# Kernel optimization log

Measured on AMD Instinct MI355X. Metric: run time of the kernel, lower is better.

The kernel has to match this reference:

```python
import jax, jax.numpy as jnp
import numpy as np

D_MODEL = 1024
NUM_HEADS = 16
SEG = 512            # segment_size
DIL = 4              # dilation_rate
HEAD_DIM = D_MODEL // NUM_HEADS


def setup_inputs() -> dict:
    key = jax.random.key(0)
    ks = jax.random.split(key, 5)
    B, S = 4, 4096
    sc = D_MODEL ** -0.5  # keep projected activations O(1) so softmax is not saturated
    def w(k):
        return jax.random.normal(k, (D_MODEL, D_MODEL), jnp.float32) * sc
    z = jnp.zeros((D_MODEL,), jnp.float32)
    return {
        "x": jax.random.normal(ks[0], (B, S, D_MODEL), jnp.float32),
        "Wq": w(ks[1]), "bq": z,
        "Wk": w(ks[2]), "bk": z,
        "Wv": w(ks[3]), "bv": z,
        "Wo": w(ks[4]), "bo": z,
    }


def reference(x, Wq, bq, Wk, bk, Wv, bv, Wo, bo):
    B, S, D = x.shape
    H, hd, seg, r = NUM_HEADS, HEAD_DIM, SEG, DIL
    scaling = hd ** -0.5

    Q = x @ Wq + bq
    K = x @ Wk + bk
    V = x @ Wv + bv

    pad = (-S) % seg
    if pad:
        Q = jnp.pad(Q, ((0, 0), (0, pad), (0, 0)))
        K = jnp.pad(K, ((0, 0), (0, pad), (0, 0)))
        V = jnp.pad(V, ((0, 0), (0, pad), (0, 0)))
    n = (S + pad) // seg          # num_segments
    sd = seg // r                 # dilated positions per segment per head

    # [B, n, sd, r, H, hd]: position within segment = t*r + offset
    def split(t):
        return t.reshape(B, n, sd, r, H, hd)

    offs = jnp.arange(H) % r      # per-head dilation offset sj = j % r
    hidx = jnp.arange(H)
    # vectorized per-head dilated gather -> [B, n, sd, H, hd]
    Qs = split(Q)[:, :, :, offs, hidx, :]
    Ks = split(K)[:, :, :, offs, hidx, :]
    Vs = split(V)[:, :, :, offs, hidx, :]

    # diagonal q.k score per dilated position, softmax over the segment's dilated positions
    scores = jnp.einsum('bnshd,bnshd->bnsh', Qs, Ks) * scaling
    probs = jax.nn.softmax(scores, axis=2)
    attn = probs[..., None] * Vs  # [B, n, sd, H, hd]

    # scatter back to each head's dilated positions; other positions stay zero
    out = jnp.zeros((B, n, sd, r, H, hd), x.dtype)
    out = out.at[:, :, :, offs, hidx, :].set(attn)
    out = out.reshape(B, n * seg, D)[:, :S]
    return out @ Wo + bo
```

## Files before the change

kernel.cpp:

```cpp
#include <hip/hip_runtime.h>
#include <hip/hip_bf16.h>

typedef unsigned short u16;
typedef unsigned int u32;
typedef __attribute__((ext_vector_type(8))) __bf16 bf16x8;
typedef __attribute__((ext_vector_type(4))) float f32x4;

#define NB 4
#define SQ 4096
#define DM 1024
#define RPC 4096
#define S4 (4 * DM)

#define VMCNT(n) asm volatile("s_waitcnt vmcnt(" #n ")" ::: "memory")
#define LGKM0()  asm volatile("s_waitcnt lgkmcnt(0)" ::: "memory")
#define BARRIER() asm volatile("s_barrier" ::: "memory")

__device__ __forceinline__ u16 f2b(float f) {
  u32 u = __builtin_bit_cast(u32, f);
  u32 r = u + 0x7fffu + ((u >> 16) & 1u);
  return (u16)(r >> 16);
}
__device__ __forceinline__ u32 cvt2(float lo, float hi) {
  u16 a = __builtin_bit_cast(u16, __float2bfloat16(lo));
  u16 b = __builtin_bit_cast(u16, __float2bfloat16(hi));
  return (u32)a | ((u32)b << 16);
}
__device__ __forceinline__ float dot2(u32 q, u32 k) {
  float ql = __builtin_bit_cast(float, q << 16);
  float qh = __builtin_bit_cast(float, q & 0xffff0000u);
  float kl = __builtin_bit_cast(float, k << 16);
  float kh = __builtin_bit_cast(float, k & 0xffff0000u);
  return ql * kl + qh * kh;
}
__device__ __forceinline__ u32 mul2(u32 v, float p) {
  float lo = __builtin_bit_cast(float, v << 16) * p;
  float hi = __builtin_bit_cast(float, v & 0xffff0000u) * p;
  return (u32)f2b(lo) | ((u32)f2b(hi) << 16);
}
__device__ __forceinline__ void gll16(const void* g, void* l) {
  __builtin_amdgcn_global_load_lds(
      (const __attribute__((address_space(1))) void*)g,
      (__attribute__((address_space(3))) void*)l, 16, 0, 0);
}

__global__ __launch_bounds__(256) void prep(const float* __restrict__ x,
                                            const float* __restrict__ Wq,
                                            const float* __restrict__ Wk,
                                            const float* __restrict__ Wv,
                                            const float* __restrict__ Wo,
                                            const float* __restrict__ bq,
                                            const float* __restrict__ bk,
                                            const float* __restrict__ bv,
                                            u16* __restrict__ xbT,
                                            u16* __restrict__ WTp,
                                            u16* __restrict__ WoTp,
                                            float* __restrict__ biasp) {
  __shared__ float T[64][65];
  const int bid = blockIdx.x;
  const int tid = threadIdx.x;
  if (bid < 1024) {
    const int wv = tid >> 6, l = tid & 63;
    const int gr0 = bid * 16 + wv * 4;
#pragma unroll
    for (int it = 0; it < 4; ++it) {
      const int gr = gr0 + it;
      const int c = gr >> 12, pr = gr & 4095;
      const int b = pr >> 10;
      const int srow = ((pr & 1023) << 2) + c;
      const int m0 = pr >> 8, rloc = pr & 255;
      const float* src = x + ((size_t)(b * SQ) + srow) * DM;
      u16* dimg = xbT + (size_t)((c * 16 + m0) * 16) * 16384 + rloc * 64;
      const int swzbase = ((((l & 15) >> 1) ^ (rloc & 7)) << 3) + (l & 1) * 4;
#pragma unroll
      for (int i = 0; i < 4; ++i) {
        float4 v = *reinterpret_cast<const float4*>(src + i * 256 + l * 4);
        uint2 pk;
        pk.x = cvt2(v.x, v.y);
        pk.y = cvt2(v.z, v.w);
        const int k64 = i * 4 + (l >> 4);
        *reinterpret_cast<uint2*>(dimg + (size_t)k64 * 16384 + swzbase) = pk;
      }
    }
  } else if (bid < 1792) {
    const int q = bid - 1024;
    const int c = q / 192;
    const int rem = q - c * 192;
    const int j0 = (rem >> 4) * 64;
    const int k0 = (rem & 15) * 64;
    const int msel = j0 >> 8;
    const float* W = (msel == 0) ? Wq : ((msel == 1) ? Wk : Wv);
    const int slot = (j0 & 255) >> 6;
    const int colbase = (c + 4 * slot) * 64;
    const int rr = tid >> 6, cc = tid & 63;
#pragma unroll
    for (int it = 0; it < 16; ++it) {
      const int kk = rr + it * 4;
      T[kk][cc] = W[(size_t)(k0 + kk) * 1024 + colbase + cc];
    }
    __syncthreads();
    const int k64 = k0 >> 6;
    const int u = cc >> 3, e = cc & 7;
#pragma unroll
    for (int it = 0; it < 16; ++it) {
      const int jj = rr + it * 4;
      const int j = j0 + jj;
      const int n0 = j / 192, nrow = j - n0 * 192;
      WTp[((size_t)((c * 4 + n0) * 16 + k64)) * 12288 + nrow * 64 + (((u ^ (nrow & 7))) << 3) + e] =
          f2b(T[cc][jj]);
    }
  } else if (bid < 2048) {
    const int q = bid - 1792;
    const int c = q >> 6;
    const int rem = q & 63;
    const int e0 = (rem >> 2) * 64;
    const int j0 = (rem & 3) * 64;
    const int rowbase = c * 64 + (j0 >> 6) * 256;
    const int rr = tid >> 6, cc = tid & 63;
#pragma unroll
    for (int it = 0; it < 16; ++it) {
      const int jj = rr + it * 4;
      T[jj][cc] = Wo[(size_t)(rowbase + jj) * 1024 + e0 + cc];
    }
    __syncthreads();
    const int k64 = j0 >> 6;
    const int u = cc >> 3, e = cc & 7;
#pragma unroll
    for (int it = 0; it < 16; ++it) {
      const int ee = rr + it * 4;
      const int n = e0 + ee;
      const int n0 = n >> 7, nrow = n & 127;
      WoTp[((size_t)((c * 8 + n0) * 4 + k64)) * 8192 + nrow * 64 + (((u ^ (nrow & 7))) << 3) + e] =
          f2b(T[cc][ee]);
    }
  } else {
    const int idx = (bid - 2048) * 256 + tid;
    if (idx < 3072) {
      const int c = idx / 768, j = idx % 768;
      const int msel = j >> 8, jj = j & 255;
      const int col = (c + 4 * (jj >> 6)) * 64 + (jj & 63);
      const float* bb = (msel == 0) ? bq : ((msel == 1) ? bk : bv);
      biasp[idx] = bb[col];
    }
  }
}

__global__ __launch_bounds__(256, 2) void gemm_qkv(const u16* __restrict__ xbT,
                                                   const u16* __restrict__ WTp,
                                                   const float* __restrict__ biasp,
                                                   u16* __restrict__ QKV) {
  __shared__ __align__(16) u16 As2[2 * 8192];
  __shared__ __align__(16) u16 Bs2[2 * 12288];
  const int p = blockIdx.x;
  const int L = (p & 7) * 64 + (p >> 3);
  const int c = L >> 7, r = L & 127;
  const int m0 = r >> 2, n0 = r & 3;
  const int tid = threadIdx.x;
  const int lane = tid & 63, w = tid >> 6;
  const int wm = w >> 1, wn = w & 1;
  const int l15 = lane & 15, l16 = lane >> 4;

  const u16* Asrc = xbT + (size_t)((c * 16 + (m0 >> 1)) * 16) * 16384 + (m0 & 1) * 8192;
  const u16* Bsrc = WTp + (size_t)((c * 4 + n0) * 16) * 12288;

  f32x4 acc[4][6];
#pragma unroll
  for (int i = 0; i < 4; ++i)
#pragma unroll
    for (int j = 0; j < 6; ++j) acc[i][j] = (f32x4){0.f, 0.f, 0.f, 0.f};

  int abase[2], bbase[2];
#pragma unroll
  for (int kk = 0; kk < 2; ++kk) {
    const int unit = kk * 4 + l16;
    abase[kk] = (wm * 64 + l15) * 64 + ((unit ^ (l15 & 7)) << 3);
    bbase[kk] = (wn * 96 + l15) * 64 + ((unit ^ (l15 & 7)) << 3);
  }

#define ISSUE_A(kt, buf)                                                   \
  {                                                                        \
    _Pragma("unroll") for (int i = 0; i < 4; ++i)                          \
        gll16(Asrc + (size_t)(kt) * 16384 + i * 2048 + tid * 8,            \
              (char*)As2 + (buf) * 16384 + i * 4096 + tid * 16);           \
  }
#define ISSUE_B(kt, buf)                                                   \
  {                                                                        \
    _Pragma("unroll") for (int i = 0; i < 6; ++i)                          \
        gll16(Bsrc + (size_t)(kt) * 12288 + i * 2048 + tid * 8,            \
              (char*)Bs2 + (buf) * 24576 + i * 4096 + tid * 16);           \
  }

  ISSUE_A(0, 0);
  ISSUE_B(0, 0);
  ISSUE_A(1, 1);
  ISSUE_B(1, 1);
  VMCNT(10);
  BARRIER();

#pragma unroll 1
  for (int t = 0; t < 16; ++t) {
    const u16* Ab = As2 + (t & 1) * 8192;
    const u16* Bb = Bs2 + (t & 1) * 12288;
#pragma unroll
    for (int kk = 0; kk < 2; ++kk) {
      bf16x8 af[4], bv[6];
#pragma unroll
      for (int mf = 0; mf < 4; ++mf)
        af[mf] = *reinterpret_cast<const bf16x8*>(Ab + abase[kk] + mf * 1024);
#pragma unroll
      for (int nf = 0; nf < 6; ++nf)
        bv[nf] = *reinterpret_cast<const bf16x8*>(Bb + bbase[kk] + nf * 1024);
      __builtin_amdgcn_s_setprio(1);
#pragma unroll
      for (int mf = 0; mf < 4; ++mf)
#pragma unroll
        for (int nf = 0; nf < 6; ++nf)
          acc[mf][nf] = __builtin_amdgcn_mfma_f32_16x16x32_bf16(af[mf], bv[nf], acc[mf][nf], 0, 0, 0);
      __builtin_amdgcn_s_setprio(0);
    }
    if (t == 15) break;
    BARRIER();
    if (t <= 13) {
      ISSUE_A(t + 2, t & 1);
      ISSUE_B(t + 2, t & 1);
      VMCNT(10);
    } else {
      VMCNT(0);
    }
    BARRIER();
  }
#undef ISSUE_A
#undef ISSUE_B

  const int rbase = m0 * 128;
  u16* outc = QKV + (size_t)c * RPC * 768;
#pragma unroll
  for (int mf = 0; mf < 4; ++mf) {
#pragma unroll
    for (int nf = 0; nf < 6; ++nf) {
      const int gcol = n0 * 192 + wn * 96 + nf * 16 + l15;
      const float bias = biasp[c * 768 + gcol];
#pragma unroll
      for (int jj = 0; jj < 4; ++jj) {
        const int rowt = wm * 64 + mf * 16 + l16 * 4 + jj;
        outc[(size_t)(rbase + rowt) * 768 + gcol] = f2b(acc[mf][nf][jj] + bias);
      }
    }
  }
}

__global__ __launch_bounds__(256, 2) void attn_out(const u16* __restrict__ QKV,
                                                   const u16* __restrict__ WoTp,
                                                   const float* __restrict__ bo,
                                                   float* __restrict__ out) {
  __shared__ __align__(16) char SMEM[67584];
  u16* As2 = (u16*)SMEM;
  u16* Bs2 = (u16*)(SMEM + 32768);
  float* pL = (float*)(SMEM + 65536);
  float* EP = (float*)SMEM;

  const int p = blockIdx.x;
  const int xcd = p & 7, idx = p >> 3;
  const int cm = xcd * 16 + (idx >> 3);
  const int n0 = idx & 7;
  const int c = cm >> 5, m0 = cm & 31;
  const int tid = threadIdx.x;
  const int lane = tid & 63, w = tid >> 6;
  const int wm = w >> 1, wn = w & 1;
  const int l15 = lane & 15, l16 = lane >> 4;

  const u16* qkv = QKV + ((size_t)c * RPC + m0 * 128) * 768;
  const u16* Bsrc = WoTp + (size_t)((c * 8 + n0) * 4) * 8192;

  {
    const int g = lane >> 3, dd = lane & 7;
#pragma unroll 4
    for (int it = 0; it < 16; ++it) {
      const int P = it * 32 + w * 8 + g;
      const int row = P >> 2, slot = P & 3;
      const u16* qp = qkv + (size_t)row * 768 + slot * 64 + dd * 8;
      uint4 qa = *reinterpret_cast<const uint4*>(qp);
      uint4 ka = *reinterpret_cast<const uint4*>(qp + 256);
      float s = dot2(qa.x, ka.x) + dot2(qa.y, ka.y) + dot2(qa.z, ka.z) + dot2(qa.w, ka.w);
      s += __shfl_xor(s, 1);
      s += __shfl_xor(s, 2);
      s += __shfl_xor(s, 4);
      if (dd == 0) pL[slot * 128 + row] = s * 0.125f;
    }
  }
  __syncthreads();

  const int vrow = tid >> 1;
  const int vq = (tid & 1) * 32;
  const u16* vsrc = qkv + (size_t)vrow * 768 + 512 + vq;
  uint4 vv0, vv1, vv2, vv3;
#define LOADV(kt)                                                          \
  {                                                                        \
    vv0 = *reinterpret_cast<const uint4*>(vsrc + (kt) * 64);               \
    vv1 = *reinterpret_cast<const uint4*>(vsrc + (kt) * 64 + 8);           \
    vv2 = *reinterpret_cast<const uint4*>(vsrc + (kt) * 64 + 16);          \
    vv3 = *reinterpret_cast<const uint4*>(vsrc + (kt) * 64 + 24);          \
  }
#define ISSUE_BO(kt, buf)                                                  \
  {                                                                        \
    _Pragma("unroll") for (int i = 0; i < 4; ++i)                          \
        gll16(Bsrc + (size_t)(kt) * 8192 + i * 2048 + tid * 8,             \
              (char*)Bs2 + (buf) * 16384 + i * 4096 + tid * 16);           \
  }
  const int aw0 = vrow * 64 + ((((tid & 1) * 4) ^ (vrow & 7)) << 3);
  const int aw1 = vrow * 64 + (((((tid & 1) * 4) + 1) ^ (vrow & 7)) << 3);
  const int aw2 = vrow * 64 + (((((tid & 1) * 4) + 2) ^ (vrow & 7)) << 3);
  const int aw3 = vrow * 64 + (((((tid & 1) * 4) + 3) ^ (vrow & 7)) << 3);
#define WRITEA(kt, buf)                                                    \
  {                                                                        \
    const float pr = pL[(kt) * 128 + vrow];                                \
    u16* ab = As2 + (buf) * 8192;                                          \
    uint4 r0, r1, r2, r3;                                                  \
    r0.x = mul2(vv0.x, pr); r0.y = mul2(vv0.y, pr);                        \
    r0.z = mul2(vv0.z, pr); r0.w = mul2(vv0.w, pr);                        \
    r1.x = mul2(vv1.x, pr); r1.y = mul2(vv1.y, pr);                        \
    r1.z = mul2(vv1.z, pr); r1.w = mul2(vv1.w, pr);                        \
    r2.x = mul2(vv2.x, pr); r2.y = mul2(vv2.y, pr);                        \
    r2.z = mul2(vv2.z, pr); r2.w = mul2(vv2.w, pr);                        \
    r3.x = mul2(vv3.x, pr); r3.y = mul2(vv3.y, pr);                        \
    r3.z = mul2(vv3.z, pr); r3.w = mul2(vv3.w, pr);                        \
    *reinterpret_cast<uint4*>(ab + aw0) = r0;                              \
    *reinterpret_cast<uint4*>(ab + aw1) = r1;                              \
    *reinterpret_cast<uint4*>(ab + aw2) = r2;                              \
    *reinterpret_cast<uint4*>(ab + aw3) = r3;                              \
  }

  LOADV(0);
  ISSUE_BO(0, 0);
  ISSUE_BO(1, 1);

  {
    float* sv = &pL[w * 128];
    const float v0 = sv[lane], v1 = sv[lane + 64];
    float m = fmaxf(v0, v1);
#pragma unroll
    for (int off = 32; off; off >>= 1) m = fmaxf(m, __shfl_xor(m, off));
    const float e0 = __expf(v0 - m), e1 = __expf(v1 - m);
    float ssum = e0 + e1;
#pragma unroll
    for (int off = 32; off; off >>= 1) ssum += __shfl_xor(ssum, off);
    const float inv = 1.f / ssum;
    sv[lane] = e0 * inv;
    sv[lane + 64] = e1 * inv;
  }
  __syncthreads();

  f32x4 acc[4][4];
#pragma unroll
  for (int i = 0; i < 4; ++i)
#pragma unroll
    for (int j = 0; j < 4; ++j) acc[i][j] = (f32x4){0.f, 0.f, 0.f, 0.f};

  int aoff[2][4], boff[2][4];
#pragma unroll
  for (int kk = 0; kk < 2; ++kk) {
    const int unit = kk * 4 + l16;
#pragma unroll
    for (int f = 0; f < 4; ++f) {
      const int ra = wm * 64 + f * 16 + l15;
      aoff[kk][f] = ra * 64 + ((unit ^ (ra & 7)) << 3);
      const int rb = wn * 64 + f * 16 + l15;
      boff[kk][f] = rb * 64 + ((unit ^ (rb & 7)) << 3);
    }
  }

  VMCNT(8);
  WRITEA(0, 0);
  LOADV(1);
  VMCNT(8);
  LGKM0();
  BARRIER();

#pragma unroll 1
  for (int t = 0; t < 4; ++t) {
    const u16* Ab = As2 + (t & 1) * 8192;
    const u16* Bb = Bs2 + (t & 1) * 8192;
#pragma unroll
    for (int kk = 0; kk < 2; ++kk) {
      bf16x8 af[4], bvv[4];
#pragma unroll
      for (int f = 0; f < 4; ++f) {
        af[f] = *reinterpret_cast<const bf16x8*>(Ab + aoff[kk][f]);
        bvv[f] = *reinterpret_cast<const bf16x8*>(Bb + boff[kk][f]);
      }
      __builtin_amdgcn_s_setprio(1);
#pragma unroll
      for (int mf = 0; mf < 4; ++mf)
#pragma unroll
        for (int nf = 0; nf < 4; ++nf)
          acc[mf][nf] = __builtin_amdgcn_mfma_f32_16x16x32_bf16(af[mf], bvv[nf], acc[mf][nf], 0, 0, 0);
      __builtin_amdgcn_s_setprio(0);
    }
    if (t == 3) break;
    BARRIER();
    if (t <= 1) {
      ISSUE_BO(t + 2, t & 1);
      VMCNT(4);
    } else {
      VMCNT(0);
    }
    WRITEA(t + 1, (t + 1) & 1);
    if (t <= 1) LOADV(t + 2);
    LGKM0();
    BARRIER();
  }
#undef LOADV
#undef ISSUE_BO
#undef WRITEA

  LGKM0();
  BARRIER();
#pragma unroll
  for (int mf = 0; mf < 4; ++mf) {
#pragma unroll
    for (int nf = 0; nf < 4; ++nf) {
      const int col = wn * 64 + nf * 16 + l15;
#pragma unroll
      for (int jj = 0; jj < 4; ++jj) {
        const int rowt = wm * 64 + mf * 16 + l16 * 4 + jj;
        EP[rowt * 130 + col] = acc[mf][nf][jj];
      }
    }
  }
  LGKM0();
  BARRIER();
  {
    const int col4 = lane & 31;
    const int rsub = lane >> 5;
    const float4 bo4 = *reinterpret_cast<const float4*>(bo + n0 * 128 + col4 * 4);
    const int rbase = m0 * 128;
    const int b = rbase >> 10;
    const int sbase = ((rbase & 1023) << 2) + c;
    float* outp = out + (size_t)(b * SQ + sbase) * DM + n0 * 128;
#pragma unroll
    for (int i = 0; i < 16; ++i) {
      const int row = w * 2 + rsub + i * 8;
      float4 v = *reinterpret_cast<const float4*>(&EP[row * 130 + col4 * 4]);
      v.x += bo4.x; v.y += bo4.y; v.z += bo4.z; v.w += bo4.w;
      *reinterpret_cast<float4*>(outp + (size_t)row * S4 + col4 * 4) = v;
    }
  }
}

extern "C" void kernel_launch(void* const* d_in, const int* in_sizes, int n_in,
                              void* d_out, int out_size, void* d_ws, size_t ws_size,
                              hipStream_t stream) {
  const float* x  = (const float*)d_in[0];
  const float* Wq = (const float*)d_in[1];
  const float* bq = (const float*)d_in[2];
  const float* Wk = (const float*)d_in[3];
  const float* bk = (const float*)d_in[4];
  const float* Wv = (const float*)d_in[5];
  const float* bv = (const float*)d_in[6];
  const float* Wo = (const float*)d_in[7];
  const float* bo = (const float*)d_in[8];
  float* out = (float*)d_out;

  char* ws = (char*)d_ws;
  u16* xbT  = (u16*)(ws);
  u16* WoTp = (u16*)(ws + 33554432);
  u16* QKV  = (u16*)(ws + 35651584);

  char* ob = (char*)d_out;
  u16*   WTp   = (u16*)(ob + 33554432);
  float* biasp = (float*)(ob + 39845888);

  prep<<<2060, 256, 0, stream>>>(x, Wq, Wk, Wv, Wo, bq, bk, bv, xbT, WTp, WoTp, biasp);
  gemm_qkv<<<512, 256, 0, stream>>>(xbT, WTp, biasp, QKV);
  attn_out<<<1024, 256, 0, stream>>>(QKV, WoTp, bo, out);
}
```

Baseline: 96.11 us.

## Retile QKV GEMM to 64x256 blocks and split output into Q, K, V planes

The QKV projection GEMM tile changes from 128x192 to 64x256, giving 768 blocks instead of 512. Each 256-wide column tile maps exactly onto Q, K or V. The epilogue now stages results in LDS and writes coalesced 16-byte rows into separate Q, K and V planes, with V stored per dilation offset so the attention kernel reads it contiguously. The weight packing is updated to match. This improves store coalescing and load locality in the attention kernel, at the cost of lower MFMA arithmetic intensity per block (re-reading A across three N tiles) and extra LDS traffic in the epilogue.

```diff
diff --git a/kernel.cpp b/kernel.cpp
--- a/kernel.cpp
+++ b/kernel.cpp
@@ -105,8 +105,8 @@
     for (int it = 0; it < 16; ++it) {
       const int jj = rr + it * 4;
       const int j = j0 + jj;
-      const int n0 = j / 192, nrow = j - n0 * 192;
-      WTp[((size_t)((c * 4 + n0) * 16 + k64)) * 12288 + nrow * 64 + (((u ^ (nrow & 7))) << 3) + e] =
+      const int n0 = j >> 8, nrow = j & 255;
+      WTp[((size_t)((c * 3 + n0) * 16 + k64)) * 16384 + nrow * 64 + (((u ^ (nrow & 7))) << 3) + e] =
           f2b(T[cc][jj]);
     }
   } else if (bid < 2048) {
@@ -148,46 +148,56 @@
 __global__ __launch_bounds__(256, 2) void gemm_qkv(const u16* __restrict__ xbT,
                                                    const u16* __restrict__ WTp,
                                                    const float* __restrict__ biasp,
-                                                   u16* __restrict__ QKV) {
-  __shared__ __align__(16) u16 As2[2 * 8192];
-  __shared__ __align__(16) u16 Bs2[2 * 12288];
+                                                   u16* __restrict__ Qp,
+                                                   u16* __restrict__ Kp,
+                                                   u16* __restrict__ Vp) {
+  __shared__ __align__(16) char SMEM[81920];
+  u16* As2 = (u16*)SMEM;
+  u16* Bs2 = (u16*)(SMEM + 16384);
+  u16* TB  = (u16*)SMEM;
+
   const int p = blockIdx.x;
-  const int L = (p & 7) * 64 + (p >> 3);
-  const int c = L >> 7, r = L & 127;
-  const int m0 = r >> 2, n0 = r & 3;
+  const int L = (p & 7) * 96 + (p >> 3);
+  const int c = L / 192;
+  const int rem = L - c * 192;
+  const int n0 = rem >> 6, m0 = rem & 63;
   const int tid = threadIdx.x;
   const int lane = tid & 63, w = tid >> 6;
-  const int wm = w >> 1, wn = w & 1;
   const int l15 = lane & 15, l16 = lane >> 4;
 
-  const u16* Asrc = xbT + (size_t)((c * 16 + (m0 >> 1)) * 16) * 16384 + (m0 & 1) * 8192;
-  const u16* Bsrc = WTp + (size_t)((c * 4 + n0) * 16) * 12288;
-
-  f32x4 acc[4][6];
+  const u16* Asrc = xbT + (size_t)((c * 16 + (m0 >> 2)) * 16) * 16384 + (m0 & 3) * 4096;
+  const u16* Bsrc = WTp + (size_t)((c * 3 + n0) * 16) * 16384;
+
+  float bias[4];
+#pragma unroll
+  for (int nf = 0; nf < 4; ++nf)
+    bias[nf] = biasp[c * 768 + n0 * 256 + w * 64 + nf * 16 + l15];
+
+  f32x4 acc[4][4];
 #pragma unroll
   for (int i = 0; i < 4; ++i)
 #pragma unroll
-    for (int j = 0; j < 6; ++j) acc[i][j] = (f32x4){0.f, 0.f, 0.f, 0.f};
+    for (int j = 0; j < 4; ++j) acc[i][j] = (f32x4){0.f, 0.f, 0.f, 0.f};
 
   int abase[2], bbase[2];
 #pragma unroll
   for (int kk = 0; kk < 2; ++kk) {
     const int unit = kk * 4 + l16;
-    abase[kk] = (wm * 64 + l15) * 64 + ((unit ^ (l15 & 7)) << 3);
-    bbase[kk] = (wn * 96 + l15) * 64 + ((unit ^ (l15 & 7)) << 3);
+    abase[kk] = l15 * 64 + ((unit ^ (l15 & 7)) << 3);
+    bbase[kk] = (w * 64 + l15) * 64 + ((unit ^ (l15 & 7)) << 3);
   }
 
 #define ISSUE_A(kt, buf)                                                   \
   {                                                                        \
-    _Pragma("unroll") for (int i = 0; i < 4; ++i)                          \
+    _Pragma("unroll") for (int i = 0; i < 2; ++i)                          \
         gll16(Asrc + (size_t)(kt) * 16384 + i * 2048 + tid * 8,            \
-              (char*)As2 + (buf) * 16384 + i * 4096 + tid * 16);           \
+              (char*)As2 + (buf) * 8192 + i * 4096 + tid * 16);            \
   }
 #define ISSUE_B(kt, buf)                                                   \
   {                                                                        \
-    _Pragma("unroll") for (int i = 0; i < 6; ++i)                          \
-        gll16(Bsrc + (size_t)(kt) * 12288 + i * 2048 + tid * 8,            \
-              (char*)Bs2 + (buf) * 24576 + i * 4096 + tid * 16);           \
+    _Pragma("unroll") for (int i = 0; i < 8; ++i)                          \
+        gll16(Bsrc + (size_t)(kt) * 16384 + i * 2048 + tid * 8,            \
+              (char*)Bs2 + (buf) * 32768 + i * 4096 + tid * 16);           \
   }
 
   ISSUE_A(0, 0);
@@ -199,22 +209,21 @@
 
 #pragma unroll 1
   for (int t = 0; t < 16; ++t) {
-    const u16* Ab = As2 + (t & 1) * 8192;
-    const u16* Bb = Bs2 + (t & 1) * 12288;
+    const u16* Ab = As2 + (t & 1) * 4096;
+    const u16* Bb = Bs2 + (t & 1) * 16384;
 #pragma unroll
     for (int kk = 0; kk < 2; ++kk) {
-      bf16x8 af[4], bv[6];
+      bf16x8 af[4], bv[4];
+#pragma unroll
+      for (int f = 0; f < 4; ++f) {
+        af[f] = *reinterpret_cast<const bf16x8*>(Ab + abase[kk] + f * 1024);
+        bv[f] = *reinterpret_cast<const bf16x8*>(Bb + bbase[kk] + f * 1024);
+      }
+      __builtin_amdgcn_s_setprio(1);
 #pragma unroll
       for (int mf = 0; mf < 4; ++mf)
-        af[mf] = *reinterpret_cast<const bf16x8*>(Ab + abase[kk] + mf * 1024);
-#pragma unroll
-      for (int nf = 0; nf < 6; ++nf)
-        bv[nf] = *reinterpret_cast<const bf16x8*>(Bb + bbase[kk] + nf * 1024);
-      __builtin_amdgcn_s_setprio(1);
-#pragma unroll
-      for (int mf = 0; mf < 4; ++mf)
-#pragma unroll
-        for (int nf = 0; nf < 6; ++nf)
+#pragma unroll
+        for (int nf = 0; nf < 4; ++nf)
           acc[mf][nf] = __builtin_amdgcn_mfma_f32_16x16x32_bf16(af[mf], bv[nf], acc[mf][nf], 0, 0, 0);
       __builtin_amdgcn_s_setprio(0);
     }
@@ -232,24 +241,43 @@
 #undef ISSUE_A
 #undef ISSUE_B
 
-  const int rbase = m0 * 128;
-  u16* outc = QKV + (size_t)c * RPC * 768;
+  LGKM0();
+  BARRIER();
 #pragma unroll
   for (int mf = 0; mf < 4; ++mf) {
 #pragma unroll
-    for (int nf = 0; nf < 6; ++nf) {
-      const int gcol = n0 * 192 + wn * 96 + nf * 16 + l15;
-      const float bias = biasp[c * 768 + gcol];
+    for (int nf = 0; nf < 4; ++nf) {
+      const int col = w * 64 + nf * 16 + l15;
 #pragma unroll
       for (int jj = 0; jj < 4; ++jj) {
-        const int rowt = wm * 64 + mf * 16 + l16 * 4 + jj;
-        outc[(size_t)(rbase + rowt) * 768 + gcol] = f2b(acc[mf][nf][jj] + bias);
+        const int row = mf * 16 + l16 * 4 + jj;
+        TB[row * 264 + col] = f2b(acc[mf][nf][jj] + bias[nf]);
       }
     }
   }
-}
-
-__global__ __launch_bounds__(256, 2) void attn_out(const u16* __restrict__ QKV,
+  LGKM0();
+  BARRIER();
+  {
+    const int row = tid >> 2, seg = tid & 3;
+    const u16* tb = TB + row * 264 + seg * 64;
+    if (n0 < 2) {
+      u16* plane = (n0 == 0) ? Qp : Kp;
+      u16* dst = plane + ((size_t)c * RPC + m0 * 64 + row) * 256 + seg * 64;
+#pragma unroll
+      for (int kk = 0; kk < 8; ++kk)
+        *reinterpret_cast<uint4*>(dst + kk * 8) = *reinterpret_cast<const uint4*>(tb + kk * 8);
+    } else {
+      u16* dst = Vp + ((size_t)(c * 4 + seg) * RPC + m0 * 64 + row) * 64;
+#pragma unroll
+      for (int kk = 0; kk < 8; ++kk)
+        *reinterpret_cast<uint4*>(dst + kk * 8) = *reinterpret_cast<const uint4*>(tb + kk * 8);
+    }
+  }
+}
+
+__global__ __launch_bounds__(256, 2) void attn_out(const u16* __restrict__ Qp,
+                                                   const u16* __restrict__ Kp,
+                                                   const u16* __restrict__ Vp,
                                                    const u16* __restrict__ WoTp,
                                                    const float* __restrict__ bo,
                                                    float* __restrict__ out) {
@@ -269,7 +297,8 @@
   const int wm = w >> 1, wn = w & 1;
   const int l15 = lane & 15, l16 = lane >> 4;
 
-  const u16* qkv = QKV + ((size_t)c * RPC + m0 * 128) * 768;
+  const u16* Qb = Qp + ((size_t)c * RPC + m0 * 128) * 256;
+  const u16* Kb = Kp + ((size_t)c * RPC + m0 * 128) * 256;
   const u16* Bsrc = WoTp + (size_t)((c * 8 + n0) * 4) * 8192;
 
   {
@@ -278,9 +307,9 @@
     for (int it = 0; it < 16; ++it) {
       const int P = it * 32 + w * 8 + g;
       const int row = P >> 2, slot = P & 3;
-      const u16* qp = qkv + (size_t)row * 768 + slot * 64 + dd * 8;
-      uint4 qa = *reinterpret_cast<const uint4*>(qp);
-      uint4 ka = *reinterpret_cast<const uint4*>(qp + 256);
+      const size_t off = (size_t)row * 256 + slot * 64 + dd * 8;
+      uint4 qa = *reinterpret_cast<const uint4*>(Qb + off);
+      uint4 ka = *reinterpret_cast<const uint4*>(Kb + off);
       float s = dot2(qa.x, ka.x) + dot2(qa.y, ka.y) + dot2(qa.z, ka.z) + dot2(qa.w, ka.w);
       s += __shfl_xor(s, 1);
       s += __shfl_xor(s, 2);
@@ -291,15 +320,15 @@
   __syncthreads();
 
   const int vrow = tid >> 1;
-  const int vq = (tid & 1) * 32;
-  const u16* vsrc = qkv + (size_t)vrow * 768 + 512 + vq;
+  const u16* vbase = Vp + ((size_t)(c * 4) * RPC + m0 * 128) * 64 + tid * 32;
   uint4 vv0, vv1, vv2, vv3;
 #define LOADV(kt)                                                          \
   {                                                                        \
-    vv0 = *reinterpret_cast<const uint4*>(vsrc + (kt) * 64);               \
-    vv1 = *reinterpret_cast<const uint4*>(vsrc + (kt) * 64 + 8);           \
-    vv2 = *reinterpret_cast<const uint4*>(vsrc + (kt) * 64 + 16);          \
-    vv3 = *reinterpret_cast<const uint4*>(vsrc + (kt) * 64 + 24);          \
+    const u16* vs = vbase + (size_t)(kt) * RPC * 64;                       \
+    vv0 = *reinterpret_cast<const uint4*>(vs);                             \
+    vv1 = *reinterpret_cast<const uint4*>(vs + 8);                         \
+    vv2 = *reinterpret_cast<const uint4*>(vs + 16);                        \
+    vv3 = *reinterpret_cast<const uint4*>(vs + 24);                        \
   }
 #define ISSUE_BO(kt, buf)                                                  \
   {                                                                        \
@@ -464,13 +493,15 @@
   char* ws = (char*)d_ws;
   u16* xbT  = (u16*)(ws);
   u16* WoTp = (u16*)(ws + 33554432);
-  u16* QKV  = (u16*)(ws + 35651584);
+  u16* Qp   = (u16*)(ws + 35651584);
+  u16* Kp   = (u16*)(ws + 44040192);
+  u16* Vp   = (u16*)(ws + 52428800);
 
   char* ob = (char*)d_out;
   u16*   WTp   = (u16*)(ob + 33554432);
   float* biasp = (float*)(ob + 39845888);
 
   prep<<<2060, 256, 0, stream>>>(x, Wq, Wk, Wv, Wo, bq, bk, bv, xbT, WTp, WoTp, biasp);
-  gemm_qkv<<<512, 256, 0, stream>>>(xbT, WTp, biasp, QKV);
-  attn_out<<<1024, 256, 0, stream>>>(QKV, WoTp, bo, out);
-}
+  gemm_qkv<<<768, 256, 0, stream>>>(xbT, WTp, biasp, Qp, Kp, Vp);
+  attn_out<<<1024, 256, 0, stream>>>(Qp, Kp, Vp, WoTp, bo, out);
+}
```

New measurement: 111.8 us. +16.3%, slower.
